# Optimization experiments

Measured on AMD Instinct MI355X. Metric: run time of the kernel, lower is better.

## Reference

```python
import jax, jax.numpy as jnp
import numpy as np

WS = 7          # window size
DISP = 3        # WS // 2 cyclic shift displacement
HEADS = 3
HD = 32         # head dim
DIM = 96        # hidden dim (= HEADS*HD)
DS = 4          # patch-merging downscale factor
NWH = 16        # windows per spatial dim after merging (112/7)
SCALE = HD ** -0.5


def _rel_indices(ws):
    idx = np.array([[x, y] for x in range(ws) for y in range(ws)])
    return idx[None, :, :] - idx[:, None, :] + ws - 1  # (ws^2, ws^2, 2)


def _shift_mask(ws, disp, nwh, nww):
    n = ws * ws
    ul = np.zeros((n, n), np.float32)
    ul[-disp * ws:, :-disp * ws] = -np.inf
    ul[:-disp * ws, -disp * ws:] = -np.inf
    lr = np.zeros((ws, ws, ws, ws), np.float32)
    lr[:, -disp:, :, :-disp] = -np.inf
    lr[:, :-disp, :, -disp:] = -np.inf
    lr = lr.reshape(n, n)
    m = np.zeros((nwh * nww, n, n), np.float32)
    m[-nww:] += ul            # last row of windows: upper/lower mask
    m[nww - 1::nww] += lr     # last column of windows: left/right mask
    return m

REL = jnp.asarray(_rel_indices(WS))                       # (49,49,2) int
SHIFT_MASK = jnp.asarray(_shift_mask(WS, DISP, NWH, NWH))  # (256,49,49)


def _layernorm(x, g, b):
    mu = jnp.mean(x, axis=-1, keepdims=True)
    var = jnp.var(x, axis=-1, keepdims=True)
    return (x - mu) * jax.lax.rsqrt(var + 1e-5) * g + b


def _window_attention(y, wqkv, pos_tab, wo, bo, shifted):
    # y: (b, nh, nw, DIM)
    if shifted:
        y = jnp.roll(y, (-DISP, -DISP), axis=(1, 2))
    b, nh, nw, _ = y.shape
    nwh, nww = nh // WS, nw // WS
    qkv = y @ wqkv  # (b, nh, nw, 3*DIM); last dim layout [q|k|v]
    qkv = qkv.reshape(b, nwh, WS, nww, WS, 3, HEADS, HD)
    qkv = qkv.transpose(5, 0, 6, 1, 3, 2, 4, 7).reshape(3, b, HEADS, nwh * nww, WS * WS, HD)
    q, k, v = qkv[0], qkv[1], qkv[2]
    dots = jnp.einsum('bhwid,bhwjd->bhwij', q, k) * SCALE  # (b,h,nwin,49,49)
    dots = dots + pos_tab[REL[..., 0], REL[..., 1]]        # relative pos bias
    if shifted:
        dots = dots + SHIFT_MASK[None, None]
    attn = jax.nn.softmax(dots, axis=-1)
    o = jnp.einsum('bhwij,bhwjd->bhwid', attn, v)
    o = o.reshape(b, HEADS, nwh, nww, WS, WS, HD)
    o = o.transpose(0, 2, 4, 3, 5, 1, 6).reshape(b, nh, nw, HEADS * HD)
    o = o @ wo + bo
    if shifted:
        o = jnp.roll(o, (DISP, DISP), axis=(1, 2))
    return o


def setup_inputs() -> dict:
    key = jax.random.key(0)
    ks = jax.random.split(key, 8)
    B, C, H, W = 16, 3, 448, 448
    s = 0.02
    return {
        'x': jax.random.normal(ks[0], (B, C, H, W), jnp.float32),
        'pm_w': jax.random.normal(ks[1], (C * DS * DS, DIM), jnp.float32) * s,
        'pm_b': jnp.zeros((DIM,), jnp.float32),
        'ln1_g': jnp.ones((2, DIM), jnp.float32),
        'ln1_b': jnp.zeros((2, DIM), jnp.float32),
        'qkv_w': jax.random.normal(ks[2], (2, DIM, 3 * HEADS * HD), jnp.float32) * s,
        'pos': jax.random.normal(ks[3], (2, 2 * WS - 1, 2 * WS - 1), jnp.float32),
        'out_w': jax.random.normal(ks[4], (2, HEADS * HD, DIM), jnp.float32) * s,
        'out_b': jnp.zeros((2, DIM), jnp.float32),
        'ln2_g': jnp.ones((2, DIM), jnp.float32),
        'ln2_b': jnp.zeros((2, DIM), jnp.float32),
        'ff1_w': jax.random.normal(ks[5], (2, DIM, 4 * DIM), jnp.float32) * s,
        'ff1_b': jnp.zeros((2, 4 * DIM), jnp.float32),
        'ff2_w': jax.random.normal(ks[6], (2, 4 * DIM, DIM), jnp.float32) * s,
        'ff2_b': jnp.zeros((2, DIM), jnp.float32),
    }


def reference(x, pm_w, pm_b, ln1_g, ln1_b, qkv_w, pos, out_w, out_b,
              ln2_g, ln2_b, ff1_w, ff1_b, ff2_w, ff2_b):
    b, c, h, w = x.shape
    # PatchMerging: Unfold(k=s=DS) orders channels as (c, kh, kw)
    xp = x.reshape(b, c, h // DS, DS, w // DS, DS)
    xp = xp.transpose(0, 2, 4, 1, 3, 5).reshape(b, h // DS, w // DS, c * DS * DS)
    xp = xp @ pm_w + pm_b  # (b, 112, 112, DIM)
    for i, shifted in enumerate((False, True)):
        y = _layernorm(xp, ln1_g[i], ln1_b[i])
        xp = xp + _window_attention(y, qkv_w[i], pos[i], out_w[i], out_b[i], shifted)
        y = _layernorm(xp, ln2_g[i], ln2_b[i])
        y = jax.nn.gelu(y @ ff1_w[i] + ff1_b[i], approximate=False) @ ff2_w[i] + ff2_b[i]
        xp = xp + y
    return xp.transpose(0, 3, 1, 2)  # (b, DIM, 112, 112)
```

## Files before the change

### kernel.cpp

```cpp
#include <hip/hip_runtime.h>
#include <hip/hip_bf16.h>

#define HW 112
#define NPIX (HW*HW)
#define NTOK_TOTAL (16*NPIX)
#define SCALE_ATTN 0.17677669529663689f

typedef short bf16x8 __attribute__((ext_vector_type(8)));
typedef float f32x4 __attribute__((ext_vector_type(4)));

__device__ __forceinline__ short f2bf(float f) {
    __hip_bfloat16 h = __float2bfloat16(f);
    return *reinterpret_cast<short*>(&h);
}

__device__ __forceinline__ float gelu_tanh(float x) {
    float t  = x * x;
    float m1 = fmaf(0.071354816f, t, 1.5957691f);
    float e  = __expf(x * m1);
    float r  = __builtin_amdgcn_rcpf(e + 1.0f);
    return fmaf(-x, r, x);
}

__global__ __launch_bounds__(256) void patch_merge_kernel(
    const float* __restrict__ x, const float* __restrict__ pm_w,
    const float* __restrict__ pm_b, float* __restrict__ xp)
{
    __shared__ float w_lds[48*96];
    __shared__ float in_lds[16*52];
    __shared__ float b_lds[96];
    const int t = threadIdx.x;
    const int jt = blockIdx.x, i = blockIdx.y, b = blockIdx.z;
    const int j0 = jt * 16;

    for (int e = t; e < 48*96; e += 256) w_lds[e] = pm_w[e];
    if (t < 96) b_lds[t] = pm_b[t];
    for (int e = t; e < 768; e += 256) {
        int r = e >> 6, col = e & 63;
        int c = r >> 2, kh = r & 3;
        float v = x[(((size_t)(b*3 + c))*448 + (4*i + kh))*448 + 4*j0 + col];
        in_lds[(col >> 2)*52 + c*16 + kh*4 + (col & 3)] = v;
    }
    __syncthreads();
    for (int e = t; e < 16*96; e += 256) {
        int pos = e / 96, ch = e % 96;
        float acc = b_lds[ch];
        #pragma unroll
        for (int k = 0; k < 48; ++k)
            acc = fmaf(in_lds[pos*52 + k], w_lds[k*96 + ch], acc);
        xp[((size_t)((b*HW + i)*HW) + j0 + pos)*96 + ch] = acc;
    }
}

__global__ __launch_bounds__(256) void prep_weights_kernel(
    const float* __restrict__ ff1, const float* __restrict__ ff2,
    const float* __restrict__ qkv_w, const float* __restrict__ out_w,
    short* __restrict__ w1T, short* __restrict__ w2T,
    short* __restrict__ qkvT, short* __restrict__ outT)
{
    int i = blockIdx.x * 256 + threadIdx.x;
    if (i < 73728) {
        int l = i / 36864, r = i % 36864, n = r / 96, k = r % 96;
        w1T[i] = f2bf(ff1[(size_t)l*36864 + k*384 + n]);
    } else if (i < 147456) {
        int j = i - 73728;
        int l = j / 36864, r = j % 36864, n = r / 384, k = r % 384;
        w2T[j] = f2bf(ff2[(size_t)l*36864 + k*96 + n]);
    } else if (i < 202752) {
        int j = i - 147456;
        int l = j / 27648, r = j % 27648, n = r / 96, k = r % 96;
        qkvT[j] = f2bf(qkv_w[(size_t)l*27648 + k*288 + n]);
    } else if (i < 221184) {
        int j = i - 202752;
        int l = j / 9216, r = j % 9216, n = r / 96, k = r % 96;
        outT[j] = f2bf(out_w[(size_t)l*9216 + k*96 + n]);
    }
}

template<bool SHIFTED>
__global__ __launch_bounds__(192) void attn_mfma_kernel(
    float* __restrict__ xp,
    const float* __restrict__ ln_g, const float* __restrict__ ln_b,
    const short* __restrict__ qkvT,
    const float* __restrict__ pos_tab,
    const short* __restrict__ outT,
    const float* __restrict__ out_b)
{
    __shared__ short bufA[13824];
    __shared__ short qk_s[13824];
    __shared__ short vT_s[6912];
    __shared__ float pos_l[169];
    __shared__ float ob_s[96];
    __shared__ float lng[96], lnb[96];

    const int t = threadIdx.x;
    const int lane = t & 63;
    const int h = t >> 6;
    const int l15 = lane & 15, lhi = lane >> 4;
    const int wh = blockIdx.x >> 4, ww = blockIdx.x & 15;
    const int b = blockIdx.y;
    const int SH = SHIFTED ? 3 : 0;

    if (t < 169) pos_l[t] = pos_tab[t];
    if (t < 96) { lng[t] = ln_g[t]; lnb[t] = ln_b[t]; ob_s[t] = out_b[t]; }
    __syncthreads();

    {
        const int part = t & 3;
        for (int row = t >> 2; row < 49; row += 48) {
            int ti = (row*37) >> 8, tj = row - ti*7;
            int gi = wh*7 + ti + SH; if (gi >= HW) gi -= HW;
            int gj = ww*7 + tj + SH; if (gj >= HW) gj -= HW;
            const float* src = xp + ((size_t)((b*HW + gi)*HW + gj))*96 + part*24;
            float v[24];
            #pragma unroll
            for (int q4 = 0; q4 < 6; ++q4) {
                float4 vv = *reinterpret_cast<const float4*>(src + q4*4);
                v[q4*4+0]=vv.x; v[q4*4+1]=vv.y; v[q4*4+2]=vv.z; v[q4*4+3]=vv.w;
            }
            float s = 0.f, s2 = 0.f;
            #pragma unroll
            for (int j = 0; j < 24; ++j) { s += v[j]; s2 += v[j]*v[j]; }
            s  += __shfl_xor(s, 1);  s  += __shfl_xor(s, 2);
            s2 += __shfl_xor(s2, 1); s2 += __shfl_xor(s2, 2);
            float mu = s * (1.f/96.f);
            float var = s2 * (1.f/96.f) - mu*mu;
            float rs = rsqrtf(var + 1e-5f);
            unsigned* yw = reinterpret_cast<unsigned*>(bufA) + row*52 + part*12;
            #pragma unroll
            for (int j = 0; j < 12; ++j) {
                int c = part*24 + 2*j;
                float lo = (v[2*j]   - mu)*rs*lng[c]   + lnb[c];
                float hi = (v[2*j+1] - mu)*rs*lng[c+1] + lnb[c+1];
                yw[j] = (unsigned)(unsigned short)f2bf(lo) |
                        ((unsigned)(unsigned short)f2bf(hi) << 16);
            }
        }
        for (int e = t; e < 15*52; e += 192)
            reinterpret_cast<unsigned*>(bufA)[(49 + e/52)*52 + e%52] = 0u;
    }
    __syncthreads();

    {
        f32x4 acc[3][2][4];
        #pragma unroll
        for (int p = 0; p < 3; ++p)
            #pragma unroll
            for (int s = 0; s < 2; ++s)
                #pragma unroll
                for (int m = 0; m < 4; ++m)
                    { acc[p][s][m][0]=0.f; acc[p][s][m][1]=0.f; acc[p][s][m][2]=0.f; acc[p][s][m][3]=0.f; }
        #pragma unroll
        for (int ks = 0; ks < 3; ++ks) {
            bf16x8 a[4];
            #pragma unroll
            for (int m = 0; m < 4; ++m)
                a[m] = *reinterpret_cast<const bf16x8*>(&bufA[(m*16 + l15)*104 + ks*32 + lhi*8]);
            #pragma unroll
            for (int p = 0; p < 3; ++p)
                #pragma unroll
                for (int s = 0; s < 2; ++s) {
                    bf16x8 bf = *reinterpret_cast<const bf16x8*>(
                        qkvT + (p*96 + h*32 + s*16 + l15)*96 + ks*32 + lhi*8);
                    #pragma unroll
                    for (int m = 0; m < 4; ++m)
                        acc[p][s][m] = __builtin_amdgcn_mfma_f32_16x16x32_bf16(
                            a[m], bf, acc[p][s][m], 0, 0, 0);
                }
        }
        #pragma unroll
        for (int p = 0; p < 3; ++p)
            #pragma unroll
            for (int s = 0; s < 2; ++s)
                #pragma unroll
                for (int m = 0; m < 4; ++m)
                    #pragma unroll
                    for (int r = 0; r < 4; ++r) {
                        int tok = m*16 + lhi*4 + r;
                        int c = s*16 + l15;
                        short val = f2bf(acc[p][s][m][r]);
                        if (p == 0)      qk_s[h*4608 + tok*72 + c] = val;
                        else if (p == 1) qk_s[h*4608 + tok*72 + 32 + c] = val;
                        else             vT_s[h*2304 + c*72 + tok] = val;
                    }
    }
    __syncthreads();

    float pv[4][4][4];
    {
        f32x4 sacc[4][4];
        #pragma unroll
        for (int m = 0; m < 4; ++m)
            #pragma unroll
            for (int n = 0; n < 4; ++n)
                { sacc[m][n][0]=0.f; sacc[m][n][1]=0.f; sacc[m][n][2]=0.f; sacc[m][n][3]=0.f; }
        bf16x8 aq[4], bk[4];
        #pragma unroll
        for (int m = 0; m < 4; ++m)
            aq[m] = *reinterpret_cast<const bf16x8*>(&qk_s[h*4608 + (m*16 + l15)*72 + lhi*8]);
        #pragma unroll
        for (int n = 0; n < 4; ++n)
            bk[n] = *reinterpret_cast<const bf16x8*>(&qk_s[h*4608 + (n*16 + l15)*72 + 32 + lhi*8]);
        #pragma unroll
        for (int m = 0; m < 4; ++m)
            #pragma unroll
            for (int n = 0; n < 4; ++n)
                sacc[m][n] = __builtin_amdgcn_mfma_f32_16x16x32_bf16(aq[m], bk[n], sacc[m][n], 0, 0, 0);

        #pragma unroll
        for (int m = 0; m < 4; ++m)
            #pragma unroll
            for (int n = 0; n < 4; ++n)
                #pragma unroll
                for (int r = 0; r < 4; ++r) {
                    int i = m*16 + lhi*4 + r, j = n*16 + l15;
                    float v;
                    if (i >= 49 || j >= 49) v = -1e30f;
                    else {
                        int xi = (i*37) >> 8, yi = i - xi*7;
                        int xj = (j*37) >> 8, yj = j - xj*7;
                        v = sacc[m][n][r]*SCALE_ATTN + pos_l[(xj - xi + 6)*13 + (yj - yi + 6)];
                        if (SHIFTED) {
                            if (wh == 15 && ((xi >= 4) != (xj >= 4))) v = -1e30f;
                            if (ww == 15 && ((yi >= 4) != (yj >= 4))) v = -1e30f;
                        }
                    }
                    pv[m][n][r] = v;
                }
    }
    #pragma unroll
    for (int m = 0; m < 4; ++m)
        #pragma unroll
        for (int r = 0; r < 4; ++r) {
            float mx = fmaxf(fmaxf(pv[m][0][r], pv[m][1][r]), fmaxf(pv[m][2][r], pv[m][3][r]));
            mx = fmaxf(mx, __shfl_xor(mx, 1)); mx = fmaxf(mx, __shfl_xor(mx, 2));
            mx = fmaxf(mx, __shfl_xor(mx, 4)); mx = fmaxf(mx, __shfl_xor(mx, 8));
            float e0 = __expf(pv[m][0][r] - mx), e1 = __expf(pv[m][1][r] - mx);
            float e2 = __expf(pv[m][2][r] - mx), e3 = __expf(pv[m][3][r] - mx);
            float s = e0 + e1 + e2 + e3;
            s += __shfl_xor(s, 1); s += __shfl_xor(s, 2);
            s += __shfl_xor(s, 4); s += __shfl_xor(s, 8);
            float inv = 1.f / s;
            pv[m][0][r] = e0*inv; pv[m][1][r] = e1*inv;
            pv[m][2][r] = e2*inv; pv[m][3][r] = e3*inv;
        }
    #pragma unroll
    for (int m = 0; m < 4; ++m)
        #pragma unroll
        for (int n = 0; n < 4; ++n)
            #pragma unroll
            for (int r = 0; r < 4; ++r)
                bufA[h*4608 + (m*16 + lhi*4 + r)*72 + n*16 + l15] = f2bf(pv[m][n][r]);

    f32x4 oacc[2][4];
    #pragma unroll
    for (int n = 0; n < 2; ++n)
        #pragma unroll
        for (int m = 0; m < 4; ++m)
            { oacc[n][m][0]=0.f; oacc[n][m][1]=0.f; oacc[n][m][2]=0.f; oacc[n][m][3]=0.f; }
    #pragma unroll
    for (int ks = 0; ks < 2; ++ks) {
        bf16x8 ap[4], bv[2];
        #pragma unroll
        for (int m = 0; m < 4; ++m)
            ap[m] = *reinterpret_cast<const bf16x8*>(&bufA[h*4608 + (m*16 + l15)*72 + ks*32 + lhi*8]);
        #pragma unroll
        for (int n = 0; n < 2; ++n)
            bv[n] = *reinterpret_cast<const bf16x8*>(&vT_s[h*2304 + (n*16 + l15)*72 + ks*32 + lhi*8]);
        #pragma unroll
        for (int n = 0; n < 2; ++n)
            #pragma unroll
            for (int m = 0; m < 4; ++m)
                oacc[n][m] = __builtin_amdgcn_mfma_f32_16x16x32_bf16(ap[m], bv[n], oacc[n][m], 0, 0, 0);
    }
    __syncthreads();
    #pragma unroll
    for (int n = 0; n < 2; ++n)
        #pragma unroll
        for (int m = 0; m < 4; ++m)
            #pragma unroll
            for (int r = 0; r < 4; ++r)
                bufA[(m*16 + lhi*4 + r)*104 + h*32 + n*16 + l15] = f2bf(oacc[n][m][r]);
    __syncthreads();

    {
        f32x4 pacc[2][4];
        #pragma unroll
        for (int n = 0; n < 2; ++n)
            #pragma unroll
            for (int m = 0; m < 4; ++m)
                { pacc[n][m][0]=0.f; pacc[n][m][1]=0.f; pacc[n][m][2]=0.f; pacc[n][m][3]=0.f; }
        #pragma unroll
        for (int ks = 0; ks < 3; ++ks) {
            bf16x8 ao[4], bw[2];
            #pragma unroll
            for (int m = 0; m < 4; ++m)
                ao[m] = *reinterpret_cast<const bf16x8*>(&bufA[(m*16 + l15)*104 + ks*32 + lhi*8]);
            #pragma unroll
            for (int n = 0; n < 2; ++n)
                bw[n] = *reinterpret_cast<const bf16x8*>(
                    outT + ((h*2 + n)*16 + l15)*96 + ks*32 + lhi*8);
            #pragma unroll
            for (int n = 0; n < 2; ++n)
                #pragma unroll
                for (int m = 0; m < 4; ++m)
                    pacc[n][m] = __builtin_amdgcn_mfma_f32_16x16x32_bf16(ao[m], bw[n], pacc[n][m], 0, 0, 0);
        }
        #pragma unroll
        for (int m = 0; m < 4; ++m)
            #pragma unroll
            for (int r = 0; r < 4; ++r) {
                int tok = m*16 + lhi*4 + r;
                if (tok < 49) {
                    int ti = (tok*37) >> 8, tj = tok - ti*7;
                    int gi = wh*7 + ti + SH; if (gi >= HW) gi -= HW;
                    int gj = ww*7 + tj + SH; if (gj >= HW) gj -= HW;
                    float* dst = xp + ((size_t)((b*HW + gi)*HW + gj))*96;
                    #pragma unroll
                    for (int n = 0; n < 2; ++n) {
                        int ch = (h*2 + n)*16 + l15;
                        dst[ch] += pacc[n][m][r] + ob_s[ch];
                    }
                }
            }
    }
}

__global__ __launch_bounds__(64, 4) void ff_mfma_kernel(
    float* __restrict__ xp,
    const float* __restrict__ ln_g, const float* __restrict__ ln_b,
    const short* __restrict__ w1T,
    const float* __restrict__ b1,
    const short* __restrict__ w2T,
    const float* __restrict__ b2)
{
    __shared__ short y_s[32*104];
    __shared__ short h_s[32*104];

    const int t = threadIdx.x;
    const int l15 = t & 15, lhi = (t & 63) >> 4;
    const size_t tok0 = (size_t)blockIdx.x * 32;

    {
        const int part = t & 3;
        const int rbase = t >> 2;
        float g[24], bb[24];
        #pragma unroll
        for (int q4 = 0; q4 < 6; ++q4) {
            float4 gv = *reinterpret_cast<const float4*>(ln_g + part*24 + q4*4);
            float4 bv = *reinterpret_cast<const float4*>(ln_b + part*24 + q4*4);
            g[q4*4+0]=gv.x; g[q4*4+1]=gv.y; g[q4*4+2]=gv.z; g[q4*4+3]=gv.w;
            bb[q4*4+0]=bv.x; bb[q4*4+1]=bv.y; bb[q4*4+2]=bv.z; bb[q4*4+3]=bv.w;
        }
        #pragma unroll
        for (int it = 0; it < 2; ++it) {
            int row = it*16 + rbase;
            const float* src = xp + (tok0 + row)*96 + part*24;
            float v[24];
            #pragma unroll
            for (int q4 = 0; q4 < 6; ++q4) {
                float4 vv = *reinterpret_cast<const float4*>(src + q4*4);
                v[q4*4+0]=vv.x; v[q4*4+1]=vv.y; v[q4*4+2]=vv.z; v[q4*4+3]=vv.w;
            }
            float s = 0.f, s2 = 0.f;
            #pragma unroll
            for (int j = 0; j < 24; ++j) { s += v[j]; s2 += v[j]*v[j]; }
            s  += __shfl_xor(s, 1);  s  += __shfl_xor(s, 2);
            s2 += __shfl_xor(s2, 1); s2 += __shfl_xor(s2, 2);
            float mu = s * (1.f/96.f);
            float var = s2 * (1.f/96.f) - mu*mu;
            float rs = rsqrtf(var + 1e-5f);
            unsigned* yw = reinterpret_cast<unsigned*>(y_s) + row*52 + part*12;
            #pragma unroll
            for (int j = 0; j < 12; ++j) {
                float lo = (v[2*j]   - mu)*rs*g[2*j]   + bb[2*j];
                float hi = (v[2*j+1] - mu)*rs*g[2*j+1] + bb[2*j+1];
                yw[j] = (unsigned)(unsigned short)f2bf(lo) |
                        ((unsigned)(unsigned short)f2bf(hi) << 16);
            }
        }
    }
    __syncthreads();

    f32x4 zero; zero[0]=0.f; zero[1]=0.f; zero[2]=0.f; zero[3]=0.f;
    f32x4 acc2[2][6];
    #pragma unroll
    for (int m = 0; m < 2; ++m)
        #pragma unroll
        for (int n = 0; n < 6; ++n) acc2[m][n] = zero;

    const int abase = l15*104 + lhi*8;

    #pragma unroll
    for (int c = 0; c < 4; ++c) {
        f32x4 acc1[2][6];
        #pragma unroll
        for (int m = 0; m < 2; ++m)
            #pragma unroll
            for (int n = 0; n < 6; ++n) acc1[m][n] = zero;
        #pragma unroll
        for (int ks = 0; ks < 3; ++ks) {
            bf16x8 a[2];
            #pragma unroll
            for (int m = 0; m < 2; ++m)
                a[m] = *reinterpret_cast<const bf16x8*>(&y_s[abase + m*16*104 + ks*32]);
            #pragma unroll
            for (int n = 0; n < 6; ++n) {
                bf16x8 bw = *reinterpret_cast<const bf16x8*>(
                    w1T + (c*96 + n*16 + l15)*96 + ks*32 + lhi*8);
                #pragma unroll
                for (int m = 0; m < 2; ++m)
                    acc1[m][n] = __builtin_amdgcn_mfma_f32_16x16x32_bf16(
                        a[m], bw, acc1[m][n], 0, 0, 0);
            }
        }

        #pragma unroll
        for (int n = 0; n < 6; ++n) {
            float bias = b1[c*96 + n*16 + l15];
            #pragma unroll
            for (int m = 0; m < 2; ++m) {
                #pragma unroll
                for (int r = 0; r < 4; ++r) {
                    float hv = gelu_tanh(acc1[m][n][r] + bias);
                    int row = m*16 + lhi*4 + r;
                    h_s[row*104 + n*16 + l15] = f2bf(hv);
                }
            }
        }

        #pragma unroll
        for (int ks = 0; ks < 3; ++ks) {
            bf16x8 a[2];
            #pragma unroll
            for (int m = 0; m < 2; ++m)
                a[m] = *reinterpret_cast<const bf16x8*>(&h_s[abase + m*16*104 + ks*32]);
            #pragma unroll
            for (int n = 0; n < 6; ++n) {
                bf16x8 bw = *reinterpret_cast<const bf16x8*>(
                    w2T + (n*16 + l15)*384 + c*96 + ks*32 + lhi*8);
                #pragma unroll
                for (int m = 0; m < 2; ++m)
                    acc2[m][n] = __builtin_amdgcn_mfma_f32_16x16x32_bf16(
                        a[m], bw, acc2[m][n], 0, 0, 0);
            }
        }
    }

    #pragma unroll
    for (int n = 0; n < 6; ++n) {
        float bias = b2[n*16 + l15];
        #pragma unroll
        for (int m = 0; m < 2; ++m) {
            #pragma unroll
            for (int r = 0; r < 4; ++r) {
                size_t row = tok0 + m*16 + lhi*4 + r;
                float* p = xp + row*96 + n*16 + l15;
                *p += acc2[m][n][r] + bias;
            }
        }
    }
}

__global__ __launch_bounds__(256) void out_kernel(
    const float* __restrict__ xp, float* __restrict__ out)
{
    __shared__ float tile[64*100];
    const int t = threadIdx.x;
    const int b = blockIdx.y;
    const int p0 = blockIdx.x * 64;
    for (int e = t; e < 64*24; e += 256) {
        int r = e / 24, p = e % 24;
        *reinterpret_cast<float4*>(&tile[r*100 + p*4]) =
            *reinterpret_cast<const float4*>(xp + ((size_t)b*NPIX + p0 + r)*96 + p*4);
    }
    __syncthreads();
    for (int e = t; e < 96*64; e += 256) {
        int ch = e >> 6, p = e & 63;
        out[((size_t)(b*96 + ch))*NPIX + p0 + p] = tile[p*100 + ch];
    }
}

extern "C" void kernel_launch(void* const* d_in, const int* in_sizes, int n_in,
                              void* d_out, int out_size, void* d_ws, size_t ws_size,
                              hipStream_t stream)
{
    (void)in_sizes; (void)n_in; (void)out_size; (void)ws_size;
    const float* x     = (const float*)d_in[0];
    const float* pm_w  = (const float*)d_in[1];
    const float* pm_b  = (const float*)d_in[2];
    const float* ln1_g = (const float*)d_in[3];
    const float* ln1_b = (const float*)d_in[4];
    const float* qkv_w = (const float*)d_in[5];
    const float* pos   = (const float*)d_in[6];
    const float* out_w = (const float*)d_in[7];
    const float* out_b = (const float*)d_in[8];
    const float* ln2_g = (const float*)d_in[9];
    const float* ln2_b = (const float*)d_in[10];
    const float* ff1_w = (const float*)d_in[11];
    const float* ff1_b = (const float*)d_in[12];
    const float* ff2_w = (const float*)d_in[13];
    const float* ff2_b = (const float*)d_in[14];

    float* xp    = (float*)d_ws;
    short* w1T_b = (short*)(xp + (size_t)NTOK_TOTAL * 96);
    short* w2T_b = w1T_b + 2*384*96;
    short* qkvT_b = w2T_b + 2*96*384;
    short* outT_b = qkvT_b + 2*288*96;

    prep_weights_kernel<<<864, 256, 0, stream>>>(ff1_w, ff2_w, qkv_w, out_w,
                                                 w1T_b, w2T_b, qkvT_b, outT_b);
    patch_merge_kernel<<<dim3(7, 112, 16), 256, 0, stream>>>(x, pm_w, pm_b, xp);

    for (int L = 0; L < 2; ++L) {
        if (L == 0)
            attn_mfma_kernel<false><<<dim3(256, 16), 192, 0, stream>>>(
                xp, ln1_g, ln1_b, qkvT_b, pos, outT_b, out_b);
        else
            attn_mfma_kernel<true><<<dim3(256, 16), 192, 0, stream>>>(
                xp, ln1_g + 96, ln1_b + 96, qkvT_b + 27648, pos + 169,
                outT_b + 9216, out_b + 96);
        ff_mfma_kernel<<<6272, 64, 0, stream>>>(
            xp, ln2_g + L*96, ln2_b + L*96,
            w1T_b + (size_t)L*384*96, ff1_b + L*384,
            w2T_b + (size_t)L*96*384, ff2_b + L*96);
    }
    out_kernel<<<dim3(196, 16), 256, 0, stream>>>(xp, (float*)d_out);
}
```

Baseline: 603.2 us.

## Restructure FF kernel as persistent blocks with double-buffered LDS weight tiles

The feed-forward kernel now launches 196 blocks of 256 threads. Each block loops over 1024 tokens and stages the FF1/FF2 weight chunks in LDS with XOR swizzling, double-buffering the next chunk through registers while the MFMAs run. Previously every 32-token block re-read weights from global/L2. LayerNorm outputs now stay in registers as MFMA A-operands, and each wave handles 64 tokens, so it issues more MFMAs per weight load. The costs are very low occupancy (196 blocks, one per CU, with large LDS and many registers) and a barrier every iteration.

```diff
diff --git a/kernel.cpp b/kernel.cpp
--- a/kernel.cpp
+++ b/kernel.cpp
@@ -326,7 +326,7 @@
     }
 }
 
-__global__ __launch_bounds__(64, 4) void ff_mfma_kernel(
+__global__ __launch_bounds__(256, 1) void ff_mfma_kernel(
     float* __restrict__ xp,
     const float* __restrict__ ln_g, const float* __restrict__ ln_b,
     const short* __restrict__ w1T,
@@ -334,131 +334,191 @@
     const short* __restrict__ w2T,
     const float* __restrict__ b2)
 {
-    __shared__ short y_s[32*104];
-    __shared__ short h_s[32*104];
+    __shared__ short wbuf[2][24576];
+    __shared__ short h_s[256*104];
 
     const int t = threadIdx.x;
-    const int l15 = t & 15, lhi = (t & 63) >> 4;
-    const size_t tok0 = (size_t)blockIdx.x * 32;
+    const int lane = t & 63;
+    const int wv = t >> 6;
+    const int l15 = lane & 15, lhi = lane >> 4;
+    const int sub = lane >> 4;
+    const int kbp = (lane & 15) * 16;
+
+    float g[24], bb[24];
+    #pragma unroll
+    for (int ks = 0; ks < 3; ++ks)
+        #pragma unroll
+        for (int q = 0; q < 2; ++q) {
+            float4 gv = *reinterpret_cast<const float4*>(ln_g + ks*32 + lhi*8 + q*4);
+            float4 bv = *reinterpret_cast<const float4*>(ln_b + ks*32 + lhi*8 + q*4);
+            g[ks*8+q*4+0]=gv.x; g[ks*8+q*4+1]=gv.y; g[ks*8+q*4+2]=gv.z; g[ks*8+q*4+3]=gv.w;
+            bb[ks*8+q*4+0]=bv.x; bb[ks*8+q*4+1]=bv.y; bb[ks*8+q*4+2]=bv.z; bb[ks*8+q*4+3]=bv.w;
+        }
 
     {
-        const int part = t & 3;
-        const int rbase = t >> 2;
-        float g[24], bb[24];
-        #pragma unroll
-        for (int q4 = 0; q4 < 6; ++q4) {
-            float4 gv = *reinterpret_cast<const float4*>(ln_g + part*24 + q4*4);
-            float4 bv = *reinterpret_cast<const float4*>(ln_b + part*24 + q4*4);
-            g[q4*4+0]=gv.x; g[q4*4+1]=gv.y; g[q4*4+2]=gv.z; g[q4*4+3]=gv.w;
-            bb[q4*4+0]=bv.x; bb[q4*4+1]=bv.y; bb[q4*4+2]=bv.z; bb[q4*4+3]=bv.w;
-        }
-        #pragma unroll
-        for (int it = 0; it < 2; ++it) {
-            int row = it*16 + rbase;
-            const float* src = xp + (tok0 + row)*96 + part*24;
-            float v[24];
-            #pragma unroll
-            for (int q4 = 0; q4 < 6; ++q4) {
-                float4 vv = *reinterpret_cast<const float4*>(src + q4*4);
-                v[q4*4+0]=vv.x; v[q4*4+1]=vv.y; v[q4*4+2]=vv.z; v[q4*4+3]=vv.w;
-            }
-            float s = 0.f, s2 = 0.f;
-            #pragma unroll
-            for (int j = 0; j < 24; ++j) { s += v[j]; s2 += v[j]*v[j]; }
-            s  += __shfl_xor(s, 1);  s  += __shfl_xor(s, 2);
-            s2 += __shfl_xor(s2, 1); s2 += __shfl_xor(s2, 2);
-            float mu = s * (1.f/96.f);
-            float var = s2 * (1.f/96.f) - mu*mu;
-            float rs = rsqrtf(var + 1e-5f);
-            unsigned* yw = reinterpret_cast<unsigned*>(y_s) + row*52 + part*12;
-            #pragma unroll
-            for (int j = 0; j < 12; ++j) {
-                float lo = (v[2*j]   - mu)*rs*g[2*j]   + bb[2*j];
-                float hi = (v[2*j+1] - mu)*rs*g[2*j+1] + bb[2*j+1];
-                yw[j] = (unsigned)(unsigned short)f2bf(lo) |
-                        ((unsigned)(unsigned short)f2bf(hi) << 16);
-            }
-        }
-    }
-    __syncthreads();
-
-    f32x4 zero; zero[0]=0.f; zero[1]=0.f; zero[2]=0.f; zero[3]=0.f;
-    f32x4 acc2[2][6];
-    #pragma unroll
-    for (int m = 0; m < 2; ++m)
-        #pragma unroll
-        for (int n = 0; n < 6; ++n) acc2[m][n] = zero;
-
-    const int abase = l15*104 + lhi*8;
-
-    #pragma unroll
-    for (int c = 0; c < 4; ++c) {
-        f32x4 acc1[2][6];
-        #pragma unroll
-        for (int m = 0; m < 2; ++m)
-            #pragma unroll
-            for (int n = 0; n < 6; ++n) acc1[m][n] = zero;
+        uint4 wreg[12];
+        #pragma unroll
+        for (int jj = 0; jj < 12; ++jj) {
+            int i = jj*4 + wv;
+            int R = i*4 + sub;
+            int kb = kbp ^ ((R & 7) << 4);
+            int kc = kb < 192 ? kb : 0;
+            const short* src = (jj < 6)
+                ? w1T + (size_t)R * 96
+                : w2T + (size_t)(R - 96) * 384;
+            wreg[jj] = *reinterpret_cast<const uint4*>(
+                reinterpret_cast<const char*>(src) + kc);
+        }
+        #pragma unroll
+        for (int jj = 0; jj < 12; ++jj) {
+            int i = jj*4 + wv;
+            *reinterpret_cast<uint4*>(&wbuf[0][i*512 + lane*8]) = wreg[jj];
+        }
+    }
+    __syncthreads();
+
+    bf16x8 y[4][3];
+    f32x4 acc2[4][6];
+    const size_t blk0 = (size_t)blockIdx.x * 1024;
+
+    for (int it = 0; it < 16; ++it) {
+        const int tt = it >> 2, c = it & 3, p = it & 1;
+        const size_t tok0 = blk0 + tt*256 + wv*64;
+
+        uint4 wreg[12];
+        {
+            const int cn = (c + 1) & 3;
+            #pragma unroll
+            for (int jj = 0; jj < 12; ++jj) {
+                int i = jj*4 + wv;
+                int R = i*4 + sub;
+                int kb = kbp ^ ((R & 7) << 4);
+                int kc = kb < 192 ? kb : 0;
+                const short* src = (jj < 6)
+                    ? w1T + (size_t)(cn*96 + R) * 96
+                    : w2T + (size_t)(R - 96) * 384 + cn*96;
+                wreg[jj] = *reinterpret_cast<const uint4*>(
+                    reinterpret_cast<const char*>(src) + kc);
+            }
+        }
+
+        if (c == 0) {
+            #pragma unroll
+            for (int m = 0; m < 4; ++m) {
+                const float* src = xp + (tok0 + m*16 + l15)*96 + lhi*8;
+                float v[24];
+                #pragma unroll
+                for (int ks = 0; ks < 3; ++ks) {
+                    float4 a0 = *reinterpret_cast<const float4*>(src + ks*32);
+                    float4 a1 = *reinterpret_cast<const float4*>(src + ks*32 + 4);
+                    v[ks*8+0]=a0.x; v[ks*8+1]=a0.y; v[ks*8+2]=a0.z; v[ks*8+3]=a0.w;
+                    v[ks*8+4]=a1.x; v[ks*8+5]=a1.y; v[ks*8+6]=a1.z; v[ks*8+7]=a1.w;
+                }
+                float s = 0.f, s2 = 0.f;
+                #pragma unroll
+                for (int j = 0; j < 24; ++j) { s += v[j]; s2 += v[j]*v[j]; }
+                s  += __shfl_xor(s, 16);  s  += __shfl_xor(s, 32);
+                s2 += __shfl_xor(s2, 16); s2 += __shfl_xor(s2, 32);
+                float mu = s * (1.f/96.f);
+                float var = s2 * (1.f/96.f) - mu*mu;
+                float rs = rsqrtf(var + 1e-5f);
+                #pragma unroll
+                for (int ks = 0; ks < 3; ++ks) {
+                    bf16x8 yy;
+                    #pragma unroll
+                    for (int j = 0; j < 8; ++j)
+                        yy[j] = f2bf((v[ks*8+j] - mu)*rs*g[ks*8+j] + bb[ks*8+j]);
+                    y[m][ks] = yy;
+                }
+            }
+            #pragma unroll
+            for (int m = 0; m < 4; ++m)
+                #pragma unroll
+                for (int n = 0; n < 6; ++n)
+                    { acc2[m][n][0]=0.f; acc2[m][n][1]=0.f; acc2[m][n][2]=0.f; acc2[m][n][3]=0.f; }
+        }
+
+        const short* w1r = wbuf[p];
+        const short* w2r = wbuf[p] + 12288;
+
+        f32x4 acc1[4][6];
+        #pragma unroll
+        for (int m = 0; m < 4; ++m)
+            #pragma unroll
+            for (int n = 0; n < 6; ++n)
+                { acc1[m][n][0]=0.f; acc1[m][n][1]=0.f; acc1[m][n][2]=0.f; acc1[m][n][3]=0.f; }
         #pragma unroll
         for (int ks = 0; ks < 3; ++ks) {
-            bf16x8 a[2];
-            #pragma unroll
-            for (int m = 0; m < 2; ++m)
-                a[m] = *reinterpret_cast<const bf16x8*>(&y_s[abase + m*16*104 + ks*32]);
+            bf16x8 bw[6];
             #pragma unroll
             for (int n = 0; n < 6; ++n) {
-                bf16x8 bw = *reinterpret_cast<const bf16x8*>(
-                    w1T + (c*96 + n*16 + l15)*96 + ks*32 + lhi*8);
-                #pragma unroll
-                for (int m = 0; m < 2; ++m)
+                int r = n*16 + l15;
+                bw[n] = *reinterpret_cast<const bf16x8*>(
+                    w1r + r*128 + ((ks*32 + lhi*8) ^ ((r & 7) << 3)));
+            }
+            #pragma unroll
+            for (int m = 0; m < 4; ++m)
+                #pragma unroll
+                for (int n = 0; n < 6; ++n)
                     acc1[m][n] = __builtin_amdgcn_mfma_f32_16x16x32_bf16(
-                        a[m], bw, acc1[m][n], 0, 0, 0);
-            }
+                        y[m][ks], bw[n], acc1[m][n], 0, 0, 0);
         }
 
         #pragma unroll
         for (int n = 0; n < 6; ++n) {
             float bias = b1[c*96 + n*16 + l15];
             #pragma unroll
-            for (int m = 0; m < 2; ++m) {
+            for (int m = 0; m < 4; ++m)
                 #pragma unroll
                 for (int r = 0; r < 4; ++r) {
                     float hv = gelu_tanh(acc1[m][n][r] + bias);
-                    int row = m*16 + lhi*4 + r;
+                    int row = wv*64 + m*16 + lhi*4 + r;
                     h_s[row*104 + n*16 + l15] = f2bf(hv);
                 }
-            }
         }
 
         #pragma unroll
         for (int ks = 0; ks < 3; ++ks) {
-            bf16x8 a[2];
-            #pragma unroll
-            for (int m = 0; m < 2; ++m)
-                a[m] = *reinterpret_cast<const bf16x8*>(&h_s[abase + m*16*104 + ks*32]);
+            bf16x8 a[4], bw[6];
+            #pragma unroll
+            for (int m = 0; m < 4; ++m)
+                a[m] = *reinterpret_cast<const bf16x8*>(
+                    &h_s[(wv*64 + m*16 + l15)*104 + ks*32 + lhi*8]);
             #pragma unroll
             for (int n = 0; n < 6; ++n) {
-                bf16x8 bw = *reinterpret_cast<const bf16x8*>(
-                    w2T + (n*16 + l15)*384 + c*96 + ks*32 + lhi*8);
-                #pragma unroll
-                for (int m = 0; m < 2; ++m)
+                int r = n*16 + l15;
+                bw[n] = *reinterpret_cast<const bf16x8*>(
+                    w2r + r*128 + ((ks*32 + lhi*8) ^ ((r & 7) << 3)));
+            }
+            #pragma unroll
+            for (int m = 0; m < 4; ++m)
+                #pragma unroll
+                for (int n = 0; n < 6; ++n)
                     acc2[m][n] = __builtin_amdgcn_mfma_f32_16x16x32_bf16(
-                        a[m], bw, acc2[m][n], 0, 0, 0);
-            }
-        }
-    }
-
-    #pragma unroll
-    for (int n = 0; n < 6; ++n) {
-        float bias = b2[n*16 + l15];
-        #pragma unroll
-        for (int m = 0; m < 2; ++m) {
-            #pragma unroll
-            for (int r = 0; r < 4; ++r) {
-                size_t row = tok0 + m*16 + lhi*4 + r;
-                float* p = xp + row*96 + n*16 + l15;
-                *p += acc2[m][n][r] + bias;
-            }
-        }
+                        a[m], bw[n], acc2[m][n], 0, 0, 0);
+        }
+
+        if (c == 3) {
+            float b2v[6];
+            #pragma unroll
+            for (int n = 0; n < 6; ++n) b2v[n] = b2[n*16 + l15];
+            #pragma unroll
+            for (int m = 0; m < 4; ++m)
+                #pragma unroll
+                for (int r = 0; r < 4; ++r) {
+                    float* dst = xp + (tok0 + m*16 + lhi*4 + r)*96 + l15;
+                    #pragma unroll
+                    for (int n = 0; n < 6; ++n)
+                        dst[n*16] += acc2[m][n][r] + b2v[n];
+                }
+        }
+
+        #pragma unroll
+        for (int jj = 0; jj < 12; ++jj) {
+            int i = jj*4 + wv;
+            *reinterpret_cast<uint4*>(&wbuf[p^1][i*512 + lane*8]) = wreg[jj];
+        }
+        __syncthreads();
     }
 }
 
@@ -520,7 +580,7 @@
             attn_mfma_kernel<true><<<dim3(256, 16), 192, 0, stream>>>(
                 xp, ln1_g + 96, ln1_b + 96, qkvT_b + 27648, pos + 169,
                 outT_b + 9216, out_b + 96);
-        ff_mfma_kernel<<<6272, 64, 0, stream>>>(
+        ff_mfma_kernel<<<196, 256, 0, stream>>>(
             xp, ln2_g + L*96, ln2_b + L*96,
             w1T_b + (size_t)L*384*96, ff1_b + L*384,
             w2T_b + (size_t)L*96*384, ff2_b + L*96);
```

Measured after the change: 765.3 us. 1.27x slower.
